# Optimization experiments

Hardware: AMD Instinct MI355X
Metric: run time of the kernel (lower is better)

Reference implementation:

```python
import jax, jax.numpy as jnp
import numpy as np

NUM_CLASSES = 90
MAX_DET_POINTS = 5000
MAX_DET_PER_IMAGE = 100
IOU_THR = 0.5
NEG = -1e10
IMAGE_SIZE = 768


def _make_anchors(image_size=IMAGE_SIZE, min_level=3, num_levels=5, anchor_scale=4.0):
    """EfficientDet-style anchors, ordered (level, y, x, anchor-config), yxyx."""
    boxes_all = []
    for li in range(num_levels):
        stride = 2 ** (min_level + li)
        boxes_level = []
        for octave in range(3):
            for aspect in (1.0, 2.0, 0.5):
                base = anchor_scale * stride * 2.0 ** (octave / 3.0)
                ax = np.sqrt(aspect)
                half_x = base * ax / 2.0
                half_y = base / ax / 2.0
                x = np.arange(stride / 2.0, image_size, stride)
                y = np.arange(stride / 2.0, image_size, stride)
                xv, yv = np.meshgrid(x, y)  # [H, W], row-major matches NHWC flatten
                xv = xv.reshape(-1)
                yv = yv.reshape(-1)
                boxes = np.stack([yv - half_y, xv - half_x, yv + half_y, xv + half_x], axis=1)
                boxes_level.append(boxes[:, None, :])
        boxes_all.append(np.concatenate(boxes_level, axis=1).reshape(-1, 4))
    return np.concatenate(boxes_all, axis=0).astype(np.float32)


def setup_inputs() -> dict:
    key = jax.random.key(0)
    ks = jax.random.split(key, 10)
    B = 8
    hw = [96, 48, 24, 12, 6]
    inp = {}
    for i, s in enumerate(hw):
        inp[f"cls{i}"] = jax.random.normal(ks[i], (B, 810, s, s), jnp.float32)
        inp[f"box{i}"] = jax.random.normal(ks[5 + i], (B, 36, s, s), jnp.float32)
    inp["anchor_boxes"] = jnp.asarray(_make_anchors())
    return inp


def _decode_boxes(rel_codes, anchors):
    # anchors: yxyx; rel_codes: (ty, tx, th, tw) -> output xyxy
    ycenter_a = (anchors[..., 0] + anchors[..., 2]) / 2
    xcenter_a = (anchors[..., 1] + anchors[..., 3]) / 2
    ha = anchors[..., 2] - anchors[..., 0]
    wa = anchors[..., 3] - anchors[..., 1]
    ty, tx, th, tw = rel_codes[..., 0], rel_codes[..., 1], rel_codes[..., 2], rel_codes[..., 3]
    w = jnp.exp(tw) * wa
    h = jnp.exp(th) * ha
    yc = ty * ha + ycenter_a
    xc = tx * wa + xcenter_a
    return jnp.stack([xc - w / 2, yc - h / 2, xc + w / 2, yc + h / 2], axis=-1)


def _nms_indices(boxes, scores, classes, iou_thr=IOU_THR, max_out=MAX_DET_PER_IMAGE):
    """torchvision.batched_nms: class-offset boxes, greedy NMS, return idx + valid mask."""
    boxes = jax.lax.stop_gradient(boxes)
    scores = jax.lax.stop_gradient(scores)
    off = classes.astype(boxes.dtype) * (jnp.max(boxes) + 1.0)
    b = boxes + off[:, None]  # [N,4]
    area = (b[:, 2] - b[:, 0]) * (b[:, 3] - b[:, 1])

    def body(i, state):
        live, sel, val = state
        idx = jnp.argmax(live)
        ok = live[idx] > 0.0  # sigmoid scores are >0; suppressed are NEG
        bi = b[idx]
        ix = jnp.maximum(0.0, jnp.minimum(b[:, 2], bi[2]) - jnp.maximum(b[:, 0], bi[0]))
        iy = jnp.maximum(0.0, jnp.minimum(b[:, 3], bi[3]) - jnp.maximum(b[:, 1], bi[1]))
        inter = ix * iy
        iou = inter / (area + area[idx] - inter + 1e-8)
        live = jnp.where(iou > iou_thr, NEG, live).at[idx].set(NEG)
        return live, sel.at[i].set(idx), val.at[i].set(ok)

    state0 = (scores, jnp.zeros((max_out,), jnp.int32), jnp.zeros((max_out,), bool))
    _, sel, val = jax.lax.fori_loop(0, max_out, body, state0)
    return sel, val


def _forward(cls_levels, box_levels, anchor_boxes):
    B = cls_levels[0].shape[0]
    C = NUM_CLASSES
    # NCHW -> NHWC -> [B, A, C] / [B, A, 4], concat over levels
    cls_all = jnp.concatenate(
        [c.transpose(0, 2, 3, 1).reshape(B, -1, C) for c in cls_levels], axis=1)
    box_all = jnp.concatenate(
        [b.transpose(0, 2, 3, 1).reshape(B, -1, 4) for b in box_levels], axis=1)

    top_vals, top_idx = jax.lax.top_k(cls_all.reshape(B, -1), MAX_DET_POINTS)
    indices = top_idx // C  # anchor index
    classes = top_idx % C
    box_topk = jnp.take_along_axis(box_all, indices[..., None], axis=1)  # [B,K,4]
    anchors_sel = anchor_boxes[indices]  # [B,K,4]

    boxes = _decode_boxes(box_topk, anchors_sel)  # xyxy [B,K,4]
    scores = jax.nn.sigmoid(top_vals)  # [B,K]

    def per_image(bx, sc, cl):
        sel, val = _nms_indices(bx, sc, cl)
        det = jnp.concatenate(
            [bx[sel], sc[sel, None], (cl[sel] + 1).astype(bx.dtype)[:, None]], axis=1)
        return jnp.where(val[:, None], det, 0.0)  # pad invalid rows with zeros

    return jax.vmap(per_image)(boxes, scores, classes)  # [B, 100, 6]


def reference(cls0, cls1, cls2, cls3, cls4, box0, box1, box2, box3, box4, anchor_boxes):
    return _forward((cls0, cls1, cls2, cls3, cls4), (box0, box1, box2, box3, box4), anchor_boxes)
```

## Files before the change

kernel.cpp:

```cpp
#include <hip/hip_runtime.h>
#include <stdint.h>

#define KDET 5000
#define MAX_OUT 100
#define PRE_THR 2.5f
#define CAND_CAP 98304u
#define SEL_N 8192u
#define TOTAL_F 9943560u
#define STAGE_CAP 1024u
#define HBINS 2048u
#define FB 0x18040u
#define CHUNKW 512u
#define SC2_CAP 2048u
#define NMSK_CAP 4096u
#define SEL_STRIDE 5120u

#define WS_CNT   0
#define WS_HIST  4096
#define WS_ZERO  69632
#define WS_META  69632
#define WS_PMAX  69760
#define WS_SELG  131072
#define WS_BX    458752
#define WS_SC    1098752
#define WS_CL    1258752
#define WS_CAND  1441792

__device__ __forceinline__ unsigned f2key(float f) {
  unsigned u = __float_as_uint(f);
  return u ^ (unsigned)(((int)u >> 31) | 0x80000000);
}

__global__ __launch_bounds__(256, 8) void scan_kernel(
    const float* __restrict__ c0, const float* __restrict__ c1,
    const float* __restrict__ c2, const float* __restrict__ c3,
    const float* __restrict__ c4,
    unsigned long long* __restrict__ cand,
    unsigned* __restrict__ cnt, unsigned* __restrict__ hist)
{
  __shared__ unsigned sh_hist[HBINS];
  __shared__ unsigned long long sh_cand[STAGE_CAP];
  __shared__ unsigned sh_ccnt;
  __shared__ unsigned sh_base;

  const unsigned img = blockIdx.y;
  const unsigned tid = threadIdx.x;
  const float* ptrs[5] = {c0, c1, c2, c3, c4};
  const unsigned lvlElems[5] = {7464960u, 1866240u, 466560u, 116640u, 29160u};
  const unsigned hw2s[5] = {9216u, 2304u, 576u, 144u, 36u};
  const unsigned fbases[5] = {0u, 7464960u, 9331200u, 9797760u, 9914400u};
  unsigned long long* candI = cand + (size_t)img * CAND_CAP;
  unsigned* histI = hist + img * HBINS;

  for (unsigned b = tid; b < HBINS; b += 256u) sh_hist[b] = 0u;
  if (tid == 0) sh_ccnt = 0u;
  __syncthreads();

#pragma unroll
  for (int lev = 0; lev < 5; ++lev) {
    const float4* p = (const float4*)(ptrs[lev] + (size_t)img * lvlElems[lev]);
    const unsigned n4 = lvlElems[lev] >> 2;
    const unsigned hw2 = hw2s[lev];
    const unsigned fbase = fbases[lev];
    const unsigned chunk = 256u * 4u;
    const unsigned sweep = gridDim.x * chunk;
    for (unsigned s0 = blockIdx.x * chunk; s0 < n4; s0 += sweep) {
      float4 v[4]; unsigned idxs[4]; bool ok[4];
#pragma unroll
      for (int u = 0; u < 4; ++u) {
        idxs[u] = s0 + (unsigned)u * 256u + tid;
        ok[u] = idxs[u] < n4;
        if (ok[u]) v[u] = p[idxs[u]];
      }
#pragma unroll
      for (int u = 0; u < 4; ++u) {
        if (!ok[u]) continue;
        float vs[4] = {v[u].x, v[u].y, v[u].z, v[u].w};
#pragma unroll
        for (int j = 0; j < 4; ++j) {
          float f = vs[j];
          if (f > PRE_THR) {
            unsigned key = f2key(f);
            unsigned bin = (key >> 15) - FB;
            if (bin > HBINS - 1u) bin = HBINS - 1u;
            atomicAdd(&sh_hist[bin], 1u);
            unsigned linear = idxs[u] * 4u + (unsigned)j;
            unsigned ch = linear / hw2;
            unsigned pos = linear - ch * hw2;
            unsigned F = fbase + pos * 810u + ch;
            unsigned slot = atomicAdd(&sh_ccnt, 1u);
            if (slot < STAGE_CAP)
              sh_cand[slot] = ((unsigned long long)key << 32) | (unsigned)(~F);
          }
        }
      }
    }
  }
  __syncthreads();

  unsigned n = sh_ccnt < STAGE_CAP ? sh_ccnt : STAGE_CAP;
  if (tid == 0) sh_base = atomicAdd(&cnt[img], n);
  __syncthreads();
  unsigned base = sh_base;
  for (unsigned k = tid; k < n; k += 256u) {
    unsigned slot = base + k;
    if (slot < CAND_CAP) candI[slot] = sh_cand[k];
  }
  for (unsigned b = tid; b < HBINS; b += 256u) {
    unsigned v = sh_hist[b];
    if (v) atomicAdd(&histI[b], v);
  }
}

__device__ __forceinline__ void bitonic_ce(unsigned long long* sb,
                                           unsigned i, unsigned ixj, bool desc) {
  unsigned long long a = sb[i], b = sb[ixj];
  if ((a < b) == desc) { sb[i] = b; sb[ixj] = a; }
}

__device__ __forceinline__ unsigned npow2(unsigned n) {
  unsigned m = 1u;
  while (m < n) m <<= 1u;
  return m;
}

__device__ void bitonic_desc(unsigned long long* a, unsigned m,
                             unsigned tid, unsigned wid, unsigned lane) {
  for (unsigned k = 2; k <= m; k <<= 1) {
    for (unsigned j = k >> 1; j; j >>= 1) {
      if (j >= 512u) {
        for (unsigned i = tid; i < m; i += 1024u) {
          unsigned ixj = i ^ j;
          if (ixj > i) bitonic_ce(a, i, ixj, (i & k) == 0);
        }
        __syncthreads();
      } else {
        unsigned base = wid * 512u;
        if (base < m) {
          unsigned lim = m - base; if (lim > 512u) lim = 512u;
#pragma unroll
          for (unsigned t = 0; t < 8; ++t) {
            unsigned io = t * 64u + lane;
            if (io < lim) {
              unsigned i = base + io;
              unsigned ixj = i ^ j;
              if (ixj > i) bitonic_ce(a, i, ixj, (i & k) == 0);
            }
          }
        }
        asm volatile("" ::: "memory");
      }
    }
    __syncthreads();
  }
}

__device__ __forceinline__ void bitonic_ce_pair(unsigned long long* kk,
                                                unsigned short* pp,
                                                unsigned i, unsigned ixj, bool desc) {
  unsigned long long a = kk[i], b = kk[ixj];
  if ((a < b) == desc) {
    kk[i] = b; kk[ixj] = a;
    unsigned short t = pp[i]; pp[i] = pp[ixj]; pp[ixj] = t;
  }
}

__device__ void bitonic_desc_pair(unsigned long long* kk, unsigned short* pp,
                                  unsigned m, unsigned tid, unsigned wid,
                                  unsigned lane) {
  for (unsigned k = 2; k <= m; k <<= 1) {
    for (unsigned j = k >> 1; j; j >>= 1) {
      if (j >= 512u) {
        for (unsigned i = tid; i < m; i += 1024u) {
          unsigned ixj = i ^ j;
          if (ixj > i) bitonic_ce_pair(kk, pp, i, ixj, (i & k) == 0);
        }
        __syncthreads();
      } else {
        unsigned base = wid * 512u;
        if (base < m) {
          unsigned lim = m - base; if (lim > 512u) lim = 512u;
#pragma unroll
          for (unsigned t = 0; t < 8; ++t) {
            unsigned io = t * 64u + lane;
            if (io < lim) {
              unsigned i = base + io;
              unsigned ixj = i ^ j;
              if (ixj > i) bitonic_ce_pair(kk, pp, i, ixj, (i & k) == 0);
            }
          }
        }
        asm volatile("" ::: "memory");
      }
    }
    __syncthreads();
  }
}

__global__ __launch_bounds__(1024) void select_kernel(
    const unsigned long long* __restrict__ cand, const unsigned* __restrict__ cnt,
    const unsigned* __restrict__ hist, unsigned long long* __restrict__ selG,
    unsigned* __restrict__ meta)
{
  const unsigned img = blockIdx.x;
  const unsigned tid = threadIdx.x;
  const unsigned wid = tid >> 6, lane = tid & 63u;
  __shared__ unsigned long long sb[SEL_N];
  __shared__ unsigned long long sc2[SC2_CAP];
  __shared__ unsigned bofs[HBINS];
  __shared__ unsigned sh_bound[16];
  __shared__ unsigned wsum[16];
  __shared__ unsigned sh_keyLow, sh_binLow, sh_SabA, sh_cntA, sh_Sab0, sh_cnt0;
  __shared__ int sh_flags;

  if (tid == 0) { sh_keyLow = 0u; sh_binLow = 0u; sh_flags = 0; }
  if (tid < 16u) sh_bound[tid] = 0u;
  for (unsigned i = tid; i < SEL_N; i += 1024u) sb[i] = 0ull;

  const unsigned* histI = hist + img * HBINS;
  unsigned b0 = 2047u - 2u * tid;
  unsigned b1 = b0 - 1u;
  unsigned h0 = histI[b0], h1 = histI[b1];
  unsigned s = h0 + h1;
  unsigned inc = s;
#pragma unroll
  for (int off = 1; off < 64; off <<= 1) {
    unsigned nv = __shfl_up(inc, off, 64);
    if ((int)lane >= off) inc += nv;
  }
  if (lane == 63u) wsum[wid] = inc;
  __syncthreads();
  if (tid < 64u) {
    unsigned v = (tid < 16u) ? wsum[tid] : 0u;
#pragma unroll
    for (int off = 1; off < 16; off <<= 1) {
      unsigned nv = __shfl_up(v, off, 64);
      if ((int)tid >= off) v += nv;
    }
    if (tid < 16u) wsum[tid] = v;
  }
  __syncthreads();
  unsigned excl = inc - s + (wid ? wsum[wid - 1] : 0u);
  bofs[b0] = excl;
  bofs[b1] = excl + h0;
  if (excl < (unsigned)KDET && excl + s >= (unsigned)KDET) {
    bool first = (excl + h0 >= (unsigned)KDET);
    unsigned binr = first ? b0 : b1;
    sh_keyLow = (binr + FB) << 15;
    sh_binLow = binr;
    sh_SabA = first ? excl : excl + h0;
    sh_cntA = first ? h0 : h1;
  }
  if (tid == 1023u) { sh_Sab0 = excl + h0; sh_cnt0 = h1; }
  __syncthreads();

  const unsigned keyLow = sh_keyLow;
  unsigned binLow, Sabove, cntLow;
  if (keyLow) { binLow = sh_binLow; Sabove = sh_SabA; cntLow = sh_cntA; }
  else        { binLow = 0u;        Sabove = sh_Sab0; cntLow = sh_cnt0; }
  const unsigned selCount = Sabove + cntLow;
  const unsigned NT = selCount < (unsigned)KDET ? selCount : (unsigned)KDET;

  {
    unsigned e0 = excl + h0;
    unsigned e1 = e0 + h1;
    if (b0 > binLow && h0 != 0u) {
      if (h0 > CHUNKW) sh_flags = 1;
      unsigned e = e0 > SEL_N ? SEL_N : e0;
      atomicMax(&sh_bound[(e - 1u) / CHUNKW], e);
    }
    if (b1 > binLow && h1 != 0u) {
      if (h1 > CHUNKW) sh_flags = 1;
      unsigned e = e1 > SEL_N ? SEL_N : e1;
      atomicMax(&sh_bound[(e - 1u) / CHUNKW], e);
    }
    if (b0 == binLow && h0 > SC2_CAP) sh_flags = 1;
    if (b1 == binLow && h1 > SC2_CAP) sh_flags = 1;
  }
  __syncthreads();

  unsigned prefEnd = sh_bound[0];
  if (sh_bound[1] > prefEnd) prefEnd = sh_bound[1];
  if (sh_bound[2] > prefEnd) prefEnd = sh_bound[2];
  if (sh_bound[3] > prefEnd) prefEnd = sh_bound[3];
  int doFull = sh_flags;
  unsigned sortedEnd;
  if (!doFull) {
    if (Sabove <= prefEnd) sortedEnd = (unsigned)KDET;
    else {
      sortedEnd = prefEnd;
      if ((unsigned)KDET - sortedEnd > NMSK_CAP) doFull = 1;
    }
  }
  if (doFull) sortedEnd = (unsigned)KDET;

  unsigned M = cnt[img]; if (M > CAND_CAP) M = CAND_CAP;
  const unsigned long long* candI = cand + (size_t)img * CAND_CAP;
  for (unsigned i = tid; i < M; i += 4096u) {
    unsigned long long c[4]; bool ok[4];
#pragma unroll
    for (int u = 0; u < 4; ++u) {
      unsigned ii = i + (unsigned)u * 1024u;
      ok[u] = ii < M;
      c[u] = ok[u] ? candI[ii] : 0ull;
    }
#pragma unroll
    for (int u = 0; u < 4; ++u) {
      if (!ok[u]) continue;
      unsigned key = (unsigned)(c[u] >> 32);
      if (key >= keyLow) {
        unsigned bin = (key >> 15) - FB;
        if (bin > HBINS - 1u) bin = HBINS - 1u;
        unsigned pos = atomicAdd(&bofs[bin], 1u);
        if (pos < SEL_N) sb[pos] = c[u];
      }
    }
  }
  __syncthreads();

  if (doFull) {
    bitonic_desc(sb, SEL_N, tid, wid, lane);
  } else {
    if (cntLow > 1u) {
      unsigned segEnd = Sabove + cntLow; if (segEnd > SEL_N) segEnd = SEL_N;
      unsigned n = segEnd - Sabove;
      if (n > 1u) {
        unsigned m = npow2(n);
        for (unsigned i = tid; i < m; i += 1024u)
          sc2[i] = (i < n) ? sb[Sabove + i] : 0ull;
        __syncthreads();
        bitonic_desc(sc2, m, tid, wid, lane);
        for (unsigned i = tid; i < n; i += 1024u) sb[Sabove + i] = sc2[i];
        __syncthreads();
      }
    }
    if (prefEnd > 1u) {
      unsigned n = prefEnd;
      unsigned m = npow2(n);
      for (unsigned i = tid; i < m; i += 1024u)
        sc2[i] = (i < n) ? sb[i] : 0ull;
      __syncthreads();
      bitonic_desc(sc2, m, tid, wid, lane);
      for (unsigned i = tid; i < n; i += 1024u) sb[i] = sc2[i];
      __syncthreads();
    }
  }

  unsigned long long* selI = selG + (size_t)img * SEL_STRIDE;
  for (unsigned i = tid; i < (unsigned)KDET; i += 1024u) selI[i] = sb[i];
  if (tid == 0) meta[img] = sortedEnd;
}

__global__ __launch_bounds__(256) void decode_kernel(
    const float* __restrict__ x0, const float* __restrict__ x1,
    const float* __restrict__ x2, const float* __restrict__ x3,
    const float* __restrict__ x4, const float* __restrict__ anchors,
    const unsigned long long* __restrict__ selG,
    float* __restrict__ bx, float* __restrict__ sc, unsigned* __restrict__ cl,
    float* __restrict__ pmax)
{
  const unsigned img = blockIdx.y;
  const unsigned blk = blockIdx.x;
  const unsigned tid = threadIdx.x;
  __shared__ float wmax[4];
  const unsigned long long* selI = selG + (size_t)img * SEL_STRIDE;
  float* bxI = bx + (size_t)img * KDET * 4;
  float* scI = sc + (size_t)img * KDET;
  unsigned* clI = cl + (size_t)img * KDET;
  const unsigned start = blk * 625u;
  const unsigned end = start + 625u;

  float lmax = -3.4e38f;
  for (unsigned e = start + tid; e < end; e += 256u) {
    unsigned long long ent = selI[e];
    unsigned keyS = (unsigned)(ent >> 32);
    unsigned F = ~(unsigned)ent;
    if (F >= TOTAL_F) F = 0u;
    unsigned ubits = (keyS & 0x80000000u) ? (keyS ^ 0x80000000u) : ~keyS;
    float logit = __uint_as_float(ubits);
    unsigned anchor = F / 90u;
    unsigned clv = F - anchor * 90u;
    const float* bp; unsigned W, ab;
    if (anchor < 82944u)       { bp = x0; W = 96; ab = 0u; }
    else if (anchor < 103680u) { bp = x1; W = 48; ab = 82944u; }
    else if (anchor < 108864u) { bp = x2; W = 24; ab = 103680u; }
    else if (anchor < 110160u) { bp = x3; W = 12; ab = 108864u; }
    else                       { bp = x4; W = 6;  ab = 110160u; }
    unsigned rel = anchor - ab;
    unsigned cell = rel / 9u;
    unsigned a = rel - cell * 9u;
    unsigned y = cell / W;
    unsigned xx = cell - y * W;
    unsigned hw2 = W * W;
    size_t baseoff = ((size_t)img * 36u + a * 4u) * hw2 + (size_t)y * W + xx;
    float ty = bp[baseoff];
    float tx = bp[baseoff + hw2];
    float th = bp[baseoff + 2 * (size_t)hw2];
    float tw = bp[baseoff + 3 * (size_t)hw2];
    float A0 = anchors[anchor * 4u + 0], A1 = anchors[anchor * 4u + 1];
    float A2 = anchors[anchor * 4u + 2], A3 = anchors[anchor * 4u + 3];
    float yca = (A0 + A2) * 0.5f;
    float xca = (A1 + A3) * 0.5f;
    float ha = A2 - A0, wa = A3 - A1;
    float w = expf(tw) * wa;
    float h = expf(th) * ha;
    float yc = ty * ha + yca;
    float xc = tx * wa + xca;
    float X1 = xc - w * 0.5f, Y1 = yc - h * 0.5f;
    float X2 = xc + w * 0.5f, Y2 = yc + h * 0.5f;
    bxI[e * 4 + 0] = X1; bxI[e * 4 + 1] = Y1; bxI[e * 4 + 2] = X2; bxI[e * 4 + 3] = Y2;
    scI[e] = 1.0f / (1.0f + expf(-logit));
    clI[e] = clv;
    lmax = fmaxf(lmax, fmaxf(fmaxf(X1, Y1), fmaxf(X2, Y2)));
  }
#pragma unroll
  for (int off = 32; off > 0; off >>= 1)
    lmax = fmaxf(lmax, __shfl_down(lmax, off, 64));
  if ((tid & 63u) == 0) wmax[tid >> 6] = lmax;
  __syncthreads();
  if (tid == 0) {
    float m = fmaxf(fmaxf(wmax[0], wmax[1]), fmaxf(wmax[2], wmax[3]));
    pmax[img * 8u + blk] = m;
  }
}

__global__ __launch_bounds__(1024) void nms_kernel(
    const float* __restrict__ bx, const float* __restrict__ sc,
    const unsigned* __restrict__ cl, const float* __restrict__ pmax,
    const unsigned long long* __restrict__ selG,
    const unsigned* __restrict__ meta,
    float* __restrict__ out)
{
  const unsigned img = blockIdx.x;
  const unsigned tid = threadIdx.x;
  const unsigned wid = tid >> 6, lane = tid & 63u;
  __shared__ float bo[KDET][4];
  __shared__ float ar[KDET];
  __shared__ unsigned long long kk[NMSK_CAP];
  __shared__ unsigned short pp[NMSK_CAP];
  __shared__ float sh_gmax;
  __shared__ float kb0[MAX_OUT], kb1[MAX_OUT], kb2[MAX_OUT], kb3[MAX_OUT], karea[MAX_OUT];
  __shared__ int sh_kidx[MAX_OUT];
  __shared__ int sh_kept;

  if (tid < 64u) {
    float v = (tid < 8u) ? pmax[img * 8u + tid] : -3.4e38f;
#pragma unroll
    for (int off = 4; off > 0; off >>= 1)
      v = fmaxf(v, __shfl_down(v, off, 64));
    if (tid == 0) sh_gmax = v;
  }
  __syncthreads();
  const float gmax1 = sh_gmax + 1.0f;
  const unsigned sortedEnd = meta[img];

  const float4* bx4 = (const float4*)(bx + (size_t)img * KDET * 4);
  const float* bxI = bx + (size_t)img * KDET * 4;
  const float* scI = sc + (size_t)img * KDET;
  const unsigned* clI = cl + (size_t)img * KDET;
  for (unsigned i = tid; i < (unsigned)KDET; i += 1024u) {
    float4 b = bx4[i];
    float offv = (float)clI[i] * gmax1;
    float X1 = b.x + offv, Y1 = b.y + offv, X2 = b.z + offv, Y2 = b.w + offv;
    bo[i][0] = X1; bo[i][1] = Y1; bo[i][2] = X2; bo[i][3] = Y2;
    ar[i] = (X2 - X1) * (Y2 - Y1);
  }
  __syncthreads();

#define NMS_STEP(ROW, KEPT) do { \
    unsigned row_ = (ROW); \
    float bjx1 = bo[row_][0], bjy1 = bo[row_][1]; \
    float bjx2 = bo[row_][2], bjy2 = bo[row_][3]; \
    float aj = ar[row_]; \
    int sup = 0; \
    for (int mI = (int)lane; mI < (KEPT); mI += 64) { \
      float ix = fmaxf(0.0f, fminf(kb2[mI], bjx2) - fmaxf(kb0[mI], bjx1)); \
      float iy = fmaxf(0.0f, fminf(kb3[mI], bjy2) - fmaxf(kb1[mI], bjy1)); \
      float inter = ix * iy; \
      float iou = inter / ((aj + karea[mI]) - inter + 1e-8f); \
      if (iou > 0.5f) sup = 1; \
    } \
    if (!__any(sup)) { \
      if (lane == 0) { \
        kb0[KEPT] = bjx1; kb1[KEPT] = bjy1; kb2[KEPT] = bjx2; kb3[KEPT] = bjy2; \
        karea[KEPT] = aj; sh_kidx[KEPT] = (int)row_; \
      } \
      (KEPT)++; \
    } \
  } while (0)

  if (tid < 64u) {
    int kept = 0;
    for (unsigned jj = 0; jj < sortedEnd && kept < MAX_OUT; ++jj)
      NMS_STEP(jj, kept);
    if (lane == 0) sh_kept = kept;
  }
  __syncthreads();

  if (sh_kept < MAX_OUT && sortedEnd < (unsigned)KDET) {
    const unsigned rem = (unsigned)KDET - sortedEnd;
    const unsigned m = npow2(rem);
    const unsigned long long* selI = selG + (size_t)img * SEL_STRIDE;
    for (unsigned i = tid; i < m; i += 1024u) {
      if (i < rem) { kk[i] = selI[sortedEnd + i]; pp[i] = (unsigned short)i; }
      else         { kk[i] = 0ull; pp[i] = 0; }
    }
    __syncthreads();
    bitonic_desc_pair(kk, pp, m, tid, wid, lane);
    if (tid < 64u) {
      int kept = sh_kept;
      for (unsigned j = 0; j < rem && kept < MAX_OUT; ++j)
        NMS_STEP(sortedEnd + (unsigned)pp[j], kept);
      if (lane == 0) sh_kept = kept;
    }
    __syncthreads();
  }

#undef NMS_STEP

  {
    const int kept = sh_kept;
    float* o = out + (size_t)img * 600;
    for (unsigned idx = tid; idx < 600u; idx += 1024u) {
      unsigned row = idx / 6u, col = idx - row * 6u;
      float v = 0.0f;
      if (row < (unsigned)kept) {
        int jj = sh_kidx[row];
        if (col < 4u)      v = bxI[jj * 4 + col];
        else if (col == 4) v = scI[jj];
        else               v = (float)(clI[jj] + 1u);
      }
      o[idx] = v;
    }
  }
}

extern "C" void kernel_launch(void* const* d_in, const int* in_sizes, int n_in,
                              void* d_out, int out_size, void* d_ws, size_t ws_size,
                              hipStream_t stream) {
  const int clsSz[5] = {59719680, 14929920, 3732480, 933120, 233280};
  const int boxSz[5] = {2654208, 663552, 165888, 41472, 10368};
  const float* cls[5] = {nullptr, nullptr, nullptr, nullptr, nullptr};
  const float* box[5] = {nullptr, nullptr, nullptr, nullptr, nullptr};
  const float* anchors = nullptr;
  for (int i = 0; i < n_in; ++i) {
    int s = in_sizes[i];
    for (int l = 0; l < 5; ++l) {
      if (s == clsSz[l]) cls[l] = (const float*)d_in[i];
      if (s == boxSz[l]) box[l] = (const float*)d_in[i];
    }
    if (s == 441936) anchors = (const float*)d_in[i];
  }
  if (!cls[0] || !box[0] || !anchors) {
    for (int l = 0; l < 5; ++l) { cls[l] = (const float*)d_in[2 * l]; box[l] = (const float*)d_in[2 * l + 1]; }
    anchors = (const float*)d_in[10];
  }

  char* ws = (char*)d_ws;
  unsigned* cnt = (unsigned*)(ws + WS_CNT);
  unsigned* hist = (unsigned*)(ws + WS_HIST);
  unsigned* metaA = (unsigned*)(ws + WS_META);
  float* pmaxA = (float*)(ws + WS_PMAX);
  unsigned long long* selG = (unsigned long long*)(ws + WS_SELG);
  float* bxA = (float*)(ws + WS_BX);
  float* scA = (float*)(ws + WS_SC);
  unsigned* clA = (unsigned*)(ws + WS_CL);
  unsigned long long* cand = (unsigned long long*)(ws + WS_CAND);

  (void)hipMemsetAsync(ws, 0, WS_ZERO, stream);
  scan_kernel<<<dim3(256, 8), 256, 0, stream>>>(
      cls[0], cls[1], cls[2], cls[3], cls[4], cand, cnt, hist);
  select_kernel<<<8, 1024, 0, stream>>>(cand, cnt, hist, selG, metaA);
  decode_kernel<<<dim3(8, 8), 256, 0, stream>>>(
      box[0], box[1], box[2], box[3], box[4], anchors, selG, bxA, scA, clA, pmaxA);
  nms_kernel<<<8, 1024, 0, stream>>>(bxA, scA, clA, pmaxA, selG, metaA,
                                     (float*)d_out);
}
```

Baseline: 541.3 us.

## Keep NMS kept-box list in registers and widen decode grid

The greedy NMS loop now stores the up to 100 kept boxes in per-lane registers (two slots per lane) instead of shared memory, and prefetches the next candidate box from shared memory one iteration early. The decode kernel is split into 16 blocks per image instead of 8, and the per-block max reduction is widened to match. This targets shared-memory latency on the serial single-wave NMS loop and the under-filled decode launch, at the cost of more registers and some predicated lane-select logic.

```diff
diff --git a/kernel.cpp b/kernel.cpp
--- a/kernel.cpp
+++ b/kernel.cpp
@@ -14,6 +14,8 @@
 #define SC2_CAP 2048u
 #define NMSK_CAP 4096u
 #define SEL_STRIDE 5120u
+#define DEC_BLKS 16u
+#define DEC_PER 313u
 
 #define WS_CNT   0
 #define WS_HIST  4096
@@ -367,8 +369,9 @@
   float* bxI = bx + (size_t)img * KDET * 4;
   float* scI = sc + (size_t)img * KDET;
   unsigned* clI = cl + (size_t)img * KDET;
-  const unsigned start = blk * 625u;
-  const unsigned end = start + 625u;
+  const unsigned start = blk * DEC_PER;
+  unsigned end = start + DEC_PER;
+  if (end > (unsigned)KDET) end = (unsigned)KDET;
 
   float lmax = -3.4e38f;
   for (unsigned e = start + tid; e < end; e += 256u) {
@@ -420,7 +423,7 @@
   __syncthreads();
   if (tid == 0) {
     float m = fmaxf(fmaxf(wmax[0], wmax[1]), fmaxf(wmax[2], wmax[3]));
-    pmax[img * 8u + blk] = m;
+    pmax[img * DEC_BLKS + blk] = m;
   }
 }
 
@@ -439,14 +442,18 @@
   __shared__ unsigned long long kk[NMSK_CAP];
   __shared__ unsigned short pp[NMSK_CAP];
   __shared__ float sh_gmax;
-  __shared__ float kb0[MAX_OUT], kb1[MAX_OUT], kb2[MAX_OUT], kb3[MAX_OUT], karea[MAX_OUT];
   __shared__ int sh_kidx[MAX_OUT];
   __shared__ int sh_kept;
 
+  float kx1[2], ky1[2], kx2[2], ky2[2], kar[2];
+  kx1[0] = kx1[1] = ky1[0] = ky1[1] = 0.0f;
+  kx2[0] = kx2[1] = ky2[0] = ky2[1] = 0.0f;
+  kar[0] = kar[1] = 0.0f;
+
   if (tid < 64u) {
-    float v = (tid < 8u) ? pmax[img * 8u + tid] : -3.4e38f;
-#pragma unroll
-    for (int off = 4; off > 0; off >>= 1)
+    float v = (tid < DEC_BLKS) ? pmax[img * DEC_BLKS + tid] : -3.4e38f;
+#pragma unroll
+    for (int off = 8; off > 0; off >>= 1)
       v = fmaxf(v, __shfl_down(v, off, 64));
     if (tid == 0) sh_gmax = v;
   }
@@ -467,33 +474,49 @@
   }
   __syncthreads();
 
-#define NMS_STEP(ROW, KEPT) do { \
-    unsigned row_ = (ROW); \
-    float bjx1 = bo[row_][0], bjy1 = bo[row_][1]; \
-    float bjx2 = bo[row_][2], bjy2 = bo[row_][3]; \
-    float aj = ar[row_]; \
+#define NMS_STEP_REG(ROWIDX, CX1, CY1, CX2, CY2, CA, KEPT) do { \
     int sup = 0; \
-    for (int mI = (int)lane; mI < (KEPT); mI += 64) { \
-      float ix = fmaxf(0.0f, fminf(kb2[mI], bjx2) - fmaxf(kb0[mI], bjx1)); \
-      float iy = fmaxf(0.0f, fminf(kb3[mI], bjy2) - fmaxf(kb1[mI], bjy1)); \
+    if ((int)lane < (KEPT)) { \
+      float ix = fmaxf(0.0f, fminf(kx2[0], (CX2)) - fmaxf(kx1[0], (CX1))); \
+      float iy = fmaxf(0.0f, fminf(ky2[0], (CY2)) - fmaxf(ky1[0], (CY1))); \
       float inter = ix * iy; \
-      float iou = inter / ((aj + karea[mI]) - inter + 1e-8f); \
-      if (iou > 0.5f) sup = 1; \
+      if (inter / (((CA) + kar[0]) - inter + 1e-8f) > 0.5f) sup = 1; \
+    } \
+    if ((int)lane + 64 < (KEPT)) { \
+      float ix = fmaxf(0.0f, fminf(kx2[1], (CX2)) - fmaxf(kx1[1], (CX1))); \
+      float iy = fmaxf(0.0f, fminf(ky2[1], (CY2)) - fmaxf(ky1[1], (CY1))); \
+      float inter = ix * iy; \
+      if (inter / (((CA) + kar[1]) - inter + 1e-8f) > 0.5f) sup = 1; \
     } \
     if (!__any(sup)) { \
-      if (lane == 0) { \
-        kb0[KEPT] = bjx1; kb1[KEPT] = bjy1; kb2[KEPT] = bjx2; kb3[KEPT] = bjy2; \
-        karea[KEPT] = aj; sh_kidx[KEPT] = (int)row_; \
+      unsigned s_ = (unsigned)(KEPT) >> 6, l_ = (unsigned)(KEPT) & 63u; \
+      if (lane == l_) { \
+        if (s_ == 0u) { kx1[0]=(CX1); ky1[0]=(CY1); kx2[0]=(CX2); ky2[0]=(CY2); kar[0]=(CA); } \
+        else          { kx1[1]=(CX1); ky1[1]=(CY1); kx2[1]=(CX2); ky2[1]=(CY2); kar[1]=(CA); } \
       } \
+      if (lane == 0u) sh_kidx[KEPT] = (int)(ROWIDX); \
       (KEPT)++; \
     } \
   } while (0)
 
+  int keptR = 0;
   if (tid < 64u) {
-    int kept = 0;
-    for (unsigned jj = 0; jj < sortedEnd && kept < MAX_OUT; ++jj)
-      NMS_STEP(jj, kept);
-    if (lane == 0) sh_kept = kept;
+    float cx1 = 0, cy1 = 0, cx2 = 0, cy2 = 0, ca = 0;
+    if (sortedEnd > 0u) {
+      cx1 = bo[0][0]; cy1 = bo[0][1]; cx2 = bo[0][2]; cy2 = bo[0][3]; ca = ar[0];
+    }
+    for (unsigned jj = 0; jj < sortedEnd && keptR < MAX_OUT; ++jj) {
+      float nx1 = 0, ny1 = 0, nx2 = 0, ny2 = 0, na = 0;
+      unsigned nj = jj + 1u;
+      bool hasN = nj < sortedEnd;
+      if (hasN) {
+        nx1 = bo[nj][0]; ny1 = bo[nj][1]; nx2 = bo[nj][2]; ny2 = bo[nj][3];
+        na = ar[nj];
+      }
+      NMS_STEP_REG(jj, cx1, cy1, cx2, cy2, ca, keptR);
+      cx1 = nx1; cy1 = ny1; cx2 = nx2; cy2 = ny2; ca = na;
+    }
+    if (lane == 0) sh_kept = keptR;
   }
   __syncthreads();
 
@@ -508,15 +531,19 @@
     __syncthreads();
     bitonic_desc_pair(kk, pp, m, tid, wid, lane);
     if (tid < 64u) {
-      int kept = sh_kept;
-      for (unsigned j = 0; j < rem && kept < MAX_OUT; ++j)
-        NMS_STEP(sortedEnd + (unsigned)pp[j], kept);
-      if (lane == 0) sh_kept = kept;
+      for (unsigned j = 0; j < rem && keptR < MAX_OUT; ++j) {
+        unsigned row = sortedEnd + (unsigned)pp[j];
+        float cx1 = bo[row][0], cy1 = bo[row][1];
+        float cx2 = bo[row][2], cy2 = bo[row][3];
+        float ca = ar[row];
+        NMS_STEP_REG(row, cx1, cy1, cx2, cy2, ca, keptR);
+      }
+      if (lane == 0) sh_kept = keptR;
     }
     __syncthreads();
   }
 
-#undef NMS_STEP
+#undef NMS_STEP_REG
 
   {
     const int kept = sh_kept;
@@ -571,7 +598,7 @@
   scan_kernel<<<dim3(256, 8), 256, 0, stream>>>(
       cls[0], cls[1], cls[2], cls[3], cls[4], cand, cnt, hist);
   select_kernel<<<8, 1024, 0, stream>>>(cand, cnt, hist, selG, metaA);
-  decode_kernel<<<dim3(8, 8), 256, 0, stream>>>(
+  decode_kernel<<<dim3(DEC_BLKS, 8), 256, 0, stream>>>(
       box[0], box[1], box[2], box[3], box[4], anchors, selG, bxA, scA, clA, pmaxA);
   nms_kernel<<<8, 1024, 0, stream>>>(bxA, scA, clA, pmaxA, selG, metaA,
                                      (float*)d_out);
```

After: 523.2 us. 3.3% less time.
